# Performance work log

Hardware: AMD Instinct MI355X
Metric: run time of the kernel (lower is better)

The kernel has to match this reference:

```python
import jax, jax.numpy as jnp
import numpy as np

DEPTH = 5
EPS = 1e-8


def setup_inputs() -> dict:
    key = jax.random.key(0)
    ks = jax.random.split(key, 7)
    N, E, Q = 50000, 1600000, 16
    return {
        "marg_i": jax.random.normal(ks[0], (N, Q), dtype=jnp.float32),
        "cav_ij": jax.random.uniform(ks[1], (E, Q), dtype=jnp.float32),
        "C": jax.random.uniform(ks[2], (Q, Q), dtype=jnp.float32),
        "field_i": jax.random.normal(ks[3], (N, Q), dtype=jnp.float32),
        "edge_dst": jax.random.randint(ks[4], (E,), 0, N, dtype=jnp.int32),
        "a1_src": jax.random.randint(ks[5], (E,), 0, N, dtype=jnp.int32),
        "indice_ij": jax.random.randint(ks[6], (E,), 0, E, dtype=jnp.int32),
    }


def reference(marg_i, cav_ij, C, field_i, edge_dst, a1_src, indice_ij):
    # Belief-propagation layers repeated DEPTH times.
    # B_ @ temp2  -> segment_sum of edge messages into destination nodes [N,Q]
    # A1 @ marg_i -> gather of source-node marginal per edge [E,Q]
    N = field_i.shape[0]

    def step(carry, _):
        marg, cav = carry
        temp2 = jnp.log(cav @ C + EPS)                                  # [E,Q]
        marg = jax.ops.segment_sum(temp2, edge_dst, num_segments=N) + field_i  # [N,Q]
        cav = jax.nn.softmax(marg[a1_src] - temp2[indice_ij], axis=1)  # [E,Q]
        return (marg, cav), None

    (marg, cav), _ = jax.lax.scan(step, (marg_i, cav_ij), None, length=DEPTH)
    return jax.nn.log_softmax(marg, axis=1)
```

## Files before the change

kernel.cpp:

```cpp
#include <hip/hip_runtime.h>
#include <hip/hip_fp16.h>

#define Q 16
#define EPS 1e-8f
#define DEPTH 5

typedef unsigned int u32;
typedef _Float16 h2 __attribute__((ext_vector_type(2)));

__device__ __forceinline__ u32 pack2(float a, float b) {
    __half2 h = __floats2half2_rn(a, b);
    return *(u32*)&h;
}
__device__ __forceinline__ float2 unpack2(u32 u) {
    __half2 h = *(__half2*)&u;
    return __half22float2(h);
}
__device__ __forceinline__ h2 mkh2(float a, float b) {
    h2 v; v[0] = (_Float16)a; v[1] = (_Float16)b; return v;
}


__global__ __launch_bounds__(256) void hist_kernel(
    const int* __restrict__ dst, int* __restrict__ count, int E)
{
    int e = blockIdx.x * 256 + threadIdx.x;
    if (e < E) atomicAdd(&count[dst[e]], 1);
}

__global__ __launch_bounds__(1024) void scan_kernel(
    const int* __restrict__ count, int* __restrict__ start, int N)
{
    __shared__ int part[1024];
    const int t = threadIdx.x;
    const int chunk = (N + 1023) / 1024;
    const int lo = t * chunk;
    const int hi = min(lo + chunk, N);

    int s = 0;
    for (int i = lo; i < hi; ++i) s += count[i];
    part[t] = s;
    __syncthreads();

    for (int off = 1; off < 1024; off <<= 1) {
        int u = (t >= off) ? part[t - off] : 0;
        __syncthreads();
        part[t] += u;
        __syncthreads();
    }

    int base = part[t] - s;
    int run = base;
    for (int i = lo; i < hi; ++i) { start[i] = run; run += count[i]; }
    if (t == 1023) start[N] = part[1023];
}

__global__ __launch_bounds__(256) void rank_kernel(
    const int* __restrict__ dst, int* __restrict__ cursor,
    int* __restrict__ pos, int E)
{
    int e = blockIdx.x * 256 + threadIdx.x;
    if (e < E) pos[e] = atomicAdd(&cursor[dst[e]], 1);
}

__global__ __launch_bounds__(256) void compose_zip(
    const int* __restrict__ a1_src, const int* __restrict__ indice,
    const int* __restrict__ dst, const int* __restrict__ pos,
    int4* __restrict__ zip, int E)
{
    int e = blockIdx.x * 256 + threadIdx.x;
    if (e < E) zip[e] = make_int4(a1_src[e], pos[indice[e]], dst[e], e);
}

__global__ __launch_bounds__(256) void scatter4(
    const int4* __restrict__ zip, const int* __restrict__ pos,
    int4* __restrict__ sorted, int E)
{
    int e = blockIdx.x * 256 + threadIdx.x;
    if (e < E) sorted[pos[e]] = zip[e];
}

__global__ __launch_bounds__(256) void meta_pack(
    const int4* __restrict__ sorted, int2* __restrict__ meta2, int E)
{
    int j = blockIdx.x * 256 + threadIdx.x;
    if (j < E) {
        int4 m = sorted[j];
        meta2[j] = make_int2(m.y, (m.z << 16) | m.x);
    }
}

template<int MODE>
__global__ __launch_bounds__(256) void fused_round(
    const int4* __restrict__ sorted, const int2* __restrict__ meta2,
    const float* __restrict__ C,
    const float* __restrict__ cav,
    const float* __restrict__ marg_in, const u32* __restrict__ t2_old,
    const int* __restrict__ start, const float* __restrict__ field,
    u32* __restrict__ t2_new, float* __restrict__ marg_out, int E)
{
    __shared__ __align__(16) h2 Csh[Q * 8];
    __shared__ float stage[256 * 17];
    __shared__ int s_nfirst, s_nlast;

    const int tid = threadIdx.x;
    const int blo = blockIdx.x * 256;
    const int bhi = min(blo + 256, E);
    if (tid < 128) {
        int q = tid >> 3, kk = tid & 7;
        Csh[q * 8 + kk] = mkh2(C[(2 * kk) * Q + q], C[(2 * kk + 1) * Q + q]);
    }
    if (tid == 0) {
        if (MODE == 0) {
            s_nfirst = sorted[blo].z;
            s_nlast  = sorted[bhi - 1].z;
        } else {
            s_nfirst = ((u32)meta2[blo].y) >> 16;
            s_nlast  = ((u32)meta2[bhi - 1].y) >> 16;
        }
    }
    __syncthreads();

    const int j = blo + tid;
    float t[Q];
    if (j < E) {
        h2 uh[8];
        float s, logs;
        if (MODE == 0) {
            const int e = sorted[j].w;
            const float4* rp = (const float4*)(cav + (size_t)e * Q);
            float4 a0 = rp[0], a1 = rp[1], a2 = rp[2], a3 = rp[3];
            uh[0] = mkh2(a0.x, a0.y); uh[1] = mkh2(a0.z, a0.w);
            uh[2] = mkh2(a1.x, a1.y); uh[3] = mkh2(a1.z, a1.w);
            uh[4] = mkh2(a2.x, a2.y); uh[5] = mkh2(a2.z, a2.w);
            uh[6] = mkh2(a3.x, a3.y); uh[7] = mkh2(a3.z, a3.w);
            s = 1.f; logs = 0.f;
        } else {
            const int2 meta = meta2[j];
            const int src = meta.y & 0xffff;
            const float4* mp = (const float4*)(marg_in + (size_t)src * Q);
            const uint4*  tp = (const uint4*)(t2_old + (size_t)meta.x * 8);
            float4 m0 = mp[0], m1 = mp[1], m2 = mp[2], m3 = mp[3];
            uint4 r0 = tp[0], r1 = tp[1];
            float2 p0 = unpack2(r0.x), p1 = unpack2(r0.y),
                   p2 = unpack2(r0.z), p3 = unpack2(r0.w);
            float2 p4 = unpack2(r1.x), p5 = unpack2(r1.y),
                   p6 = unpack2(r1.z), p7 = unpack2(r1.w);

            float x[Q] = {m0.x - p0.x, m0.y - p0.y, m0.z - p1.x, m0.w - p1.y,
                          m1.x - p2.x, m1.y - p2.y, m1.z - p3.x, m1.w - p3.y,
                          m2.x - p4.x, m2.y - p4.y, m2.z - p5.x, m2.w - p5.y,
                          m3.x - p6.x, m3.y - p6.y, m3.z - p7.x, m3.w - p7.y};

            float mx = x[0];
#pragma unroll
            for (int q = 1; q < Q; ++q) mx = fmaxf(mx, x[q]);
            float u[Q];
            s = 0.f;
#pragma unroll
            for (int q = 0; q < Q; ++q) { u[q] = __expf(x[q] - mx); s += u[q]; }
            logs = __logf(s);
#pragma unroll
            for (int k = 0; k < 8; ++k) uh[k] = mkh2(u[2 * k], u[2 * k + 1]);
        }

        const float base = EPS * s;
#pragma unroll
        for (int q = 0; q < Q; ++q) {
            const uint4* cp = (const uint4*)&Csh[q * 8];
            h2 col[8];
            ((uint4*)col)[0] = cp[0];
            ((uint4*)col)[1] = cp[1];
            float acc = base;
#pragma unroll
            for (int kk = 0; kk < 8; ++kk)
                acc = __builtin_amdgcn_fdot2(uh[kk], col[kk], acc, false);
            t[q] = __logf(acc) - logs;
        }

        if (MODE != 2) {
            uint4 w0, w1;
            w0.x = pack2(t[0],  t[1]);  w0.y = pack2(t[2],  t[3]);
            w0.z = pack2(t[4],  t[5]);  w0.w = pack2(t[6],  t[7]);
            w1.x = pack2(t[8],  t[9]);  w1.y = pack2(t[10], t[11]);
            w1.z = pack2(t[12], t[13]); w1.w = pack2(t[14], t[15]);
            uint4* op = (uint4*)(t2_new + (size_t)j * 8);
            op[0] = w0; op[1] = w1;
        }
    } else {
#pragma unroll
        for (int q = 0; q < Q; ++q) t[q] = 0.f;
    }

#pragma unroll
    for (int q = 0; q < Q; ++q) stage[tid * 17 + q] = t[q];
    __syncthreads();

    const int nfirst = s_nfirst;
    const int ncnt = s_nlast - nfirst + 1;
    for (int k = tid; k < ncnt * Q; k += 256) {
        int ln = k >> 4, q = k & 15;
        int n = nfirst + ln;
        int slo = start[n], shi = start[n + 1];
        int lo = max(slo, blo), hi = min(shi, bhi);
        float s = 0.f;
        for (int sl = lo; sl < hi; ++sl) s += stage[(sl - blo) * 17 + q];
        if (slo >= blo && shi <= bhi)
            marg_out[(size_t)n * Q + q] = s + field[(size_t)n * Q + q];
        else
            atomicAdd(marg_out + (size_t)n * Q + q, s);
    }
}

__global__ __launch_bounds__(256) void node_out(
    const float* __restrict__ marg, float* __restrict__ out, int N)
{
    int i = blockIdx.x * 256 + threadIdx.x;
    if (i >= N) return;

    const float4* mp = (const float4*)(marg + (size_t)i * Q);
    float4 m0 = mp[0], m1 = mp[1], m2 = mp[2], m3 = mp[3];
    float x[Q] = {m0.x, m0.y, m0.z, m0.w, m1.x, m1.y, m1.z, m1.w,
                  m2.x, m2.y, m2.z, m2.w, m3.x, m3.y, m3.z, m3.w};

    float mx = x[0];
#pragma unroll
    for (int q = 1; q < Q; ++q) mx = fmaxf(mx, x[q]);
    float s = 0.f;
#pragma unroll
    for (int q = 0; q < Q; ++q) s += __expf(x[q] - mx);
    float lse = mx + __logf(s);

    float4* op = (float4*)(out + (size_t)i * Q);
    op[0] = make_float4(x[0]  - lse, x[1]  - lse, x[2]  - lse, x[3]  - lse);
    op[1] = make_float4(x[4]  - lse, x[5]  - lse, x[6]  - lse, x[7]  - lse);
    op[2] = make_float4(x[8]  - lse, x[9]  - lse, x[10] - lse, x[11] - lse);
    op[3] = make_float4(x[12] - lse, x[13] - lse, x[14] - lse, x[15] - lse);
}

extern "C" void kernel_launch(void* const* d_in, const int* in_sizes, int n_in,
                              void* d_out, int out_size, void* d_ws, size_t ws_size,
                              hipStream_t stream) {
    const float* cav_in   = (const float*)d_in[1];
    const float* C        = (const float*)d_in[2];
    const float* field_i  = (const float*)d_in[3];
    const int*   edge_dst = (const int*)d_in[4];
    const int*   a1_src   = (const int*)d_in[5];
    const int*   indice   = (const int*)d_in[6];
    float* out = (float*)d_out;

    const int E = in_sizes[4];
    const int N = in_sizes[0] / Q;

    char* ws = (char*)d_ws;
    const size_t t2_bytes   = (size_t)E * 32;
    const size_t i4_bytes   = (size_t)E * 16;
    const size_t node_bytes = (size_t)N * Q * sizeof(float);
    u32*   t2a    = (u32*)ws;                     ws += t2_bytes;
    u32*   t2b    = (u32*)ws;                     ws += t2_bytes;
    int4*  zip    = (int4*)ws;                    ws += i4_bytes;
    int4*  sorted = (int4*)ws;                    ws += i4_bytes;
    int2*  meta2  = (int2*)ws;                    ws += (size_t)E * 8;
    float* marg_a = (float*)ws;                   ws += node_bytes;
    float* marg_b = (float*)ws;                   ws += node_bytes;
    int*   pos    = (int*)ws;                     ws += (size_t)E * 4;
    int*   count  = (int*)ws;                     ws += (size_t)N * 4;
    int*   start  = (int*)ws;                     ws += (size_t)(N + 1) * 4;
    int*   cursor = (int*)ws;

    const int eb = 256;
    const int eg = (E + eb - 1) / eb;
    const int ng = (N + eb - 1) / eb;

    hipMemsetAsync(count, 0, (size_t)N * 4, stream);
    hist_kernel<<<eg, eb, 0, stream>>>(edge_dst, count, E);
    scan_kernel<<<1, 1024, 0, stream>>>(count, start, N);
    hipMemcpyAsync(cursor, start, (size_t)N * 4, hipMemcpyDeviceToDevice, stream);
    rank_kernel<<<eg, eb, 0, stream>>>(edge_dst, cursor, pos, E);
    compose_zip<<<eg, eb, 0, stream>>>(a1_src, indice, edge_dst, pos, zip, E);
    scatter4<<<eg, eb, 0, stream>>>(zip, pos, sorted, E);
    meta_pack<<<eg, eb, 0, stream>>>(sorted, meta2, E);

    u32* t_cur = t2a;
    u32* t_nxt = t2b;
    float* m_in = marg_b;
    float* m_out = marg_a;

    for (int it = 0; it < DEPTH; ++it) {
        hipMemcpyAsync(m_out, field_i, node_bytes, hipMemcpyDeviceToDevice, stream);
        if (it == 0)
            fused_round<0><<<eg, eb, 0, stream>>>(sorted, meta2, C, cav_in,
                                                  nullptr, nullptr, start, field_i,
                                                  t_cur, m_out, E);
        else if (it != DEPTH - 1)
            fused_round<1><<<eg, eb, 0, stream>>>(sorted, meta2, C, nullptr,
                                                  m_in, t_cur, start, field_i,
                                                  t_nxt, m_out, E);
        else
            fused_round<2><<<eg, eb, 0, stream>>>(sorted, meta2, C, nullptr,
                                                  m_in, t_cur, start, field_i,
                                                  nullptr, m_out, E);
        if (it != 0) { u32* tt = t_cur; t_cur = t_nxt; t_nxt = tt; }
        float* tm = m_in; m_in = m_out; m_out = tm;
    }

    node_out<<<ng, eb, 0, stream>>>(m_in, out, N);
}
```

Before: 732.0 us.

## Parallelize CSR scan and only initialize boundary-spanning nodes with field

Replaces the single-block serial-chunk prefix scan with a three-pass multi-block scan. Instead of copying the full field array into the marginal buffer every round, builds a list of nodes that are empty or whose edge segment crosses a 256-edge block boundary and initializes only those. This relies on the fused kernel writing non-boundary nodes directly, so only atomically accumulated nodes need pre-seeding. It adds two small kernels and an atomic list build, and correctness depends on fused_round's boundary handling matching this criterion.

```diff
diff --git a/kernel.cpp b/kernel.cpp
--- a/kernel.cpp
+++ b/kernel.cpp
@@ -28,31 +28,55 @@
     if (e < E) atomicAdd(&count[dst[e]], 1);
 }
 
-__global__ __launch_bounds__(1024) void scan_kernel(
-    const int* __restrict__ count, int* __restrict__ start, int N)
-{
-    __shared__ int part[1024];
-    const int t = threadIdx.x;
-    const int chunk = (N + 1023) / 1024;
-    const int lo = t * chunk;
-    const int hi = min(lo + chunk, N);
-
-    int s = 0;
-    for (int i = lo; i < hi; ++i) s += count[i];
-    part[t] = s;
-    __syncthreads();
-
+__global__ __launch_bounds__(256) void scan_partial(
+    const int* __restrict__ count, int* __restrict__ partial, int N)
+{
+    __shared__ int sm[256];
+    int i = blockIdx.x * 256 + threadIdx.x;
+    sm[threadIdx.x] = (i < N) ? count[i] : 0;
+    __syncthreads();
+    for (int off = 128; off > 0; off >>= 1) {
+        if (threadIdx.x < off) sm[threadIdx.x] += sm[threadIdx.x + off];
+        __syncthreads();
+    }
+    if (threadIdx.x == 0) partial[blockIdx.x] = sm[0];
+}
+
+__global__ __launch_bounds__(1024) void scan_top(
+    int* __restrict__ partial, int nb)
+{
+    __shared__ int sm[1024];
+    int t = threadIdx.x;
+    int v = (t < nb) ? partial[t] : 0;
+    sm[t] = v;
+    __syncthreads();
     for (int off = 1; off < 1024; off <<= 1) {
-        int u = (t >= off) ? part[t - off] : 0;
-        __syncthreads();
-        part[t] += u;
-        __syncthreads();
-    }
-
-    int base = part[t] - s;
-    int run = base;
-    for (int i = lo; i < hi; ++i) { start[i] = run; run += count[i]; }
-    if (t == 1023) start[N] = part[1023];
+        int u = (t >= off) ? sm[t - off] : 0;
+        __syncthreads();
+        sm[t] += u;
+        __syncthreads();
+    }
+    if (t < nb) partial[t] = sm[t] - v;
+}
+
+__global__ __launch_bounds__(256) void scan_final(
+    const int* __restrict__ count, const int* __restrict__ partial,
+    int* __restrict__ start, int N)
+{
+    __shared__ int sm[256];
+    int i = blockIdx.x * 256 + threadIdx.x;
+    int v = (i < N) ? count[i] : 0;
+    sm[threadIdx.x] = v;
+    __syncthreads();
+    for (int off = 1; off < 256; off <<= 1) {
+        int u = (threadIdx.x >= off) ? sm[threadIdx.x - off] : 0;
+        __syncthreads();
+        sm[threadIdx.x] += u;
+        __syncthreads();
+    }
+    int excl = sm[threadIdx.x] - v + partial[blockIdx.x];
+    if (i < N) start[i] = excl;
+    if (i == N - 1) start[N] = excl + v;
 }
 
 __global__ __launch_bounds__(256) void rank_kernel(
@@ -88,6 +112,32 @@
         int4 m = sorted[j];
         meta2[j] = make_int2(m.y, (m.z << 16) | m.x);
     }
+}
+
+__global__ __launch_bounds__(256) void bnode_build(
+    const int* __restrict__ start, int* __restrict__ blist,
+    int* __restrict__ bcount, int N)
+{
+    int n = blockIdx.x * 256 + threadIdx.x;
+    if (n >= N) return;
+    int slo = start[n], shi = start[n + 1];
+    bool need = (slo == shi) || ((slo >> 8) != ((shi - 1) >> 8));
+    if (need) {
+        int p = atomicAdd(bcount, 1);
+        blist[p] = n;
+    }
+}
+
+__global__ __launch_bounds__(256) void binit(
+    const int* __restrict__ blist, const int* __restrict__ bcount,
+    const float* __restrict__ field, float* __restrict__ marg)
+{
+    int idx = blockIdx.x * 256 + threadIdx.x;
+    int cnt = *bcount;
+    if (idx >= cnt * 4) return;
+    int n = blist[idx >> 2], part = idx & 3;
+    ((float4*)(marg + (size_t)n * Q))[part] =
+        ((const float4*)(field + (size_t)n * Q))[part];
 }
 
 template<int MODE>
@@ -265,29 +315,36 @@
     float* marg_b = (float*)ws;                   ws += node_bytes;
     int*   pos    = (int*)ws;                     ws += (size_t)E * 4;
     int*   count  = (int*)ws;                     ws += (size_t)N * 4;
+    int*   bcount = (int*)ws;                     ws += 4;
     int*   start  = (int*)ws;                     ws += (size_t)(N + 1) * 4;
-    int*   cursor = (int*)ws;
+    int*   cursor = (int*)ws;                     ws += (size_t)N * 4;
+    int*   blist  = (int*)ws;                     ws += (size_t)N * 4;
+    int*   partial= (int*)ws;
 
     const int eb = 256;
     const int eg = (E + eb - 1) / eb;
     const int ng = (N + eb - 1) / eb;
 
-    hipMemsetAsync(count, 0, (size_t)N * 4, stream);
+    hipMemsetAsync(count, 0, (size_t)N * 4 + 4, stream);
     hist_kernel<<<eg, eb, 0, stream>>>(edge_dst, count, E);
-    scan_kernel<<<1, 1024, 0, stream>>>(count, start, N);
+    scan_partial<<<ng, eb, 0, stream>>>(count, partial, N);
+    scan_top<<<1, 1024, 0, stream>>>(partial, ng);
+    scan_final<<<ng, eb, 0, stream>>>(count, partial, start, N);
     hipMemcpyAsync(cursor, start, (size_t)N * 4, hipMemcpyDeviceToDevice, stream);
     rank_kernel<<<eg, eb, 0, stream>>>(edge_dst, cursor, pos, E);
     compose_zip<<<eg, eb, 0, stream>>>(a1_src, indice, edge_dst, pos, zip, E);
     scatter4<<<eg, eb, 0, stream>>>(zip, pos, sorted, E);
     meta_pack<<<eg, eb, 0, stream>>>(sorted, meta2, E);
+    bnode_build<<<ng, eb, 0, stream>>>(start, blist, bcount, N);
 
     u32* t_cur = t2a;
     u32* t_nxt = t2b;
     float* m_in = marg_b;
     float* m_out = marg_a;
+    const int bg = (N * 4 + eb - 1) / eb;
 
     for (int it = 0; it < DEPTH; ++it) {
-        hipMemcpyAsync(m_out, field_i, node_bytes, hipMemcpyDeviceToDevice, stream);
+        binit<<<bg, eb, 0, stream>>>(blist, bcount, field_i, m_out);
         if (it == 0)
             fused_round<0><<<eg, eb, 0, stream>>>(sorted, meta2, C, cav_in,
                                                   nullptr, nullptr, start, field_i,
```

Result: faster. 666.5 us (-8.9%).
